# Performance work log

Hardware: AMD Instinct MI355X
Metric: run time of the kernel (lower is better)

Reference implementation:

```python
import jax, jax.numpy as jnp
import numpy as np

NUM_CLASSES = 91
BBOX_XFORM_CLIP = float(np.log(1000.0 / 16.0))
WX, WY, WW, WH = 10.0, 10.0, 5.0, 5.0  # torchvision BoxCoder weights
DETECTIONS_PER_IMG = 100


def _decode_boxes(reg, props):
    # reg: [P, 4*C], props: [P, 4] -> [P, C, 4]  (torchvision BoxCoder.decode)
    widths = props[:, 2] - props[:, 0]
    heights = props[:, 3] - props[:, 1]
    ctr_x = props[:, 0] + 0.5 * widths
    ctr_y = props[:, 1] + 0.5 * heights
    r = reg.reshape(reg.shape[0], -1, 4)
    dx = r[..., 0] / WX
    dy = r[..., 1] / WY
    dw = jnp.minimum(r[..., 2] / WW, BBOX_XFORM_CLIP)
    dh = jnp.minimum(r[..., 3] / WH, BBOX_XFORM_CLIP)
    pcx = dx * widths[:, None] + ctr_x[:, None]
    pcy = dy * heights[:, None] + ctr_y[:, None]
    pw = jnp.exp(dw) * widths[:, None]
    ph = jnp.exp(dh) * heights[:, None]
    return jnp.stack([pcx - 0.5 * pw, pcy - 0.5 * ph, pcx + 0.5 * pw, pcy + 0.5 * ph], axis=-1)


def _clip_boxes(boxes, h, w):
    x = jnp.clip(boxes[..., 0::2], 0.0, float(w))
    y = jnp.clip(boxes[..., 1::2], 0.0, float(h))
    return jnp.stack([x[..., 0], y[..., 0], x[..., 1], y[..., 1]], axis=-1)


def setup_inputs() -> dict:
    key = jax.random.key(0)
    k1, k2, k3, k4, k5 = jax.random.split(key, 5)
    B, P, C, FD = 8, 4096, NUM_CLASSES, 1024
    N = B * P
    class_logits = jax.random.normal(k1, (N, C), dtype=jnp.float32)
    box_regression = 0.5 * jax.random.normal(k2, (N, 4 * C), dtype=jnp.float32)
    # valid proposal boxes inside an 800x800 image: x1<x2, y1<y2
    xy = jax.random.uniform(k3, (N, 2), dtype=jnp.float32) * 700.0
    wh = jax.random.uniform(k4, (N, 2), dtype=jnp.float32) * 96.0 + 4.0
    proposals = jnp.concatenate([xy, xy + wh], axis=-1)
    box_features = jax.random.normal(k5, (N, FD), dtype=jnp.float32)
    return {"class_logits": class_logits, "box_regression": box_regression,
            "proposals": proposals, "box_features": box_features,
            "batch_size": B, "image_h": 800, "image_w": 800}


def reference(class_logits, box_regression, proposals, box_features, batch_size, image_h, image_w):
    B = int(batch_size)
    N = class_logits.shape[0]
    P = N // B
    lg = class_logits.reshape(B, P, NUM_CLASSES)
    rg = box_regression.reshape(B, P, 4 * NUM_CLASSES)
    pr = proposals.reshape(B, P, 4)
    ft = box_features.reshape(B, P, -1)

    def per_image(lg_i, rg_i, pr_i, ft_i):
        boxes = _decode_boxes(rg_i, pr_i)            # [P, C, 4]
        scores = jax.nn.softmax(lg_i, axis=-1)       # [P, C]
        boxes = _clip_boxes(boxes, image_h, image_w)
        boxes = boxes[:, 1:].reshape(-1, 4)          # drop background class -> [P*(C-1), 4]
        scores = scores[:, 1:].reshape(-1)
        # batched_nms with iou_threshold=1.0 never suppresses anything (IoU<=1 always),
        # so keep == indices sorted by score descending, truncated to detections_per_img.
        keep = jnp.argsort(-scores)[:DETECTIONS_PER_IMG]
        boxes = boxes / float(image_h)               # source divides by image_shape[0] only
        kept_boxes = boxes[keep]                     # [D, 4]
        feat_idx = keep // (NUM_CLASSES - 1)         # source: keep / (num_classes-1) int div
        kept_feats = ft_i[feat_idx]                  # [D, FD]
        return kept_boxes, kept_feats

    all_boxes, all_features = jax.vmap(per_image)(lg, rg, pr, ft)
    return all_boxes, all_features
```

## Files before the change

### kernel.cpp

```cpp
#include <hip/hip_runtime.h>
#include <hip/hip_bf16.h>

#define NCLS 91
#define NFG 90
#define NDET 100
#define FDIM 1024
#define CAP 4096
#define NBUK 4096
#define BBOX_CLIP 4.135166556742356f
#define RPB 32

__global__ void k_zero(unsigned* __restrict__ p, int n) {
    int i = blockIdx.x * 256 + threadIdx.x;
    if (i < n) p[i] = 0u;
}

__global__ __launch_bounds__(256) void k_softhist(const float* __restrict__ logits,
                                                  float* __restrict__ rowoff,
                                                  unsigned* __restrict__ ghist, int P) {
    __shared__ unsigned h[NBUK];
    for (int b = threadIdx.x; b < NBUK; b += 256) h[b] = 0u;
    __syncthreads();
    int bpi = (P + RPB - 1) / RPB;
    int img = blockIdx.x / bpi;
    int blk = blockIdx.x % bpi;
    int wave = threadIdx.x >> 6, lane = threadIdx.x & 63;
    #pragma unroll
    for (int it = 0; it < RPB / 4; it++) {
        int rl = blk * RPB + it * 4 + wave;
        if (rl >= P) break;
        long long row = (long long)img * P + rl;
        const float* r = logits + row * NCLS;
        float l1 = r[lane];
        float l2 = (lane < NCLS - 64) ? r[64 + lane] : -INFINITY;
        float m = fmaxf(l1, l2);
        #pragma unroll
        for (int o = 32; o; o >>= 1) m = fmaxf(m, __shfl_xor(m, o));
        float e = expf(l1 - m) + ((lane < NCLS - 64) ? expf(l2 - m) : 0.0f);
        #pragma unroll
        for (int o = 32; o; o >>= 1) e += __shfl_xor(e, o);
        float off = m + logf(e);
        if (lane == 0) rowoff[row] = off;
        if (lane >= 1) {
            unsigned k1 = __float_as_uint(expf(l1 - off));
            atomicAdd(&h[k1 >> 20], 1u);
        }
        if (lane < NCLS - 64) {
            unsigned k2 = __float_as_uint(expf(l2 - off));
            atomicAdd(&h[k2 >> 20], 1u);
        }
    }
    __syncthreads();
    for (int b = threadIdx.x; b < NBUK; b += 256)
        if (h[b]) atomicAdd(&ghist[img * NBUK + b], h[b]);
}

__global__ void k_threshold(const unsigned* __restrict__ ghist,
                            unsigned* __restrict__ lowBound) {
    __shared__ unsigned partial[256];
    __shared__ unsigned suffix[257];
    int img = blockIdx.x;
    const unsigned* h = ghist + img * NBUK;
    unsigned local[16];
    unsigned sum = 0;
    #pragma unroll
    for (int i = 0; i < 16; i++) { local[i] = h[threadIdx.x * 16 + i]; sum += local[i]; }
    partial[threadIdx.x] = sum;
    __syncthreads();
    if (threadIdx.x == 0) {
        unsigned run = 0;
        suffix[256] = 0;
        for (int t = 255; t >= 0; t--) { run += partial[t]; suffix[t] = run; }
    }
    __syncthreads();
    unsigned run = suffix[threadIdx.x + 1];
    #pragma unroll
    for (int i = 15; i >= 0; i--) {
        unsigned prev = run;
        run += local[i];
        if (run >= NDET && prev < NDET)
            lowBound[img] = ((unsigned)(threadIdx.x * 16 + i)) << 20;
    }
}

__global__ void k_collect(const float* __restrict__ logits,
                          const float* __restrict__ rowoff,
                          const unsigned* __restrict__ lowBound,
                          unsigned* __restrict__ gcnt,
                          unsigned long long* __restrict__ cand, int P, int bpi) {
    int img = blockIdx.x / bpi;
    int blk = blockIdx.x % bpi;
    unsigned lb = lowBound[img];
    int base = blk * 4096;
    int rowbase = img * P;
    int elems = P * NFG;
    #pragma unroll
    for (int i = 0; i < 16; i++) {
        int e = base + i * 256 + threadIdx.x;
        if (e < elems) {
            int p = e / NFG, cm = e - p * NFG;
            long long rr = rowbase + p;
            float sc = expf(logits[rr * NCLS + cm + 1] - rowoff[rr]);
            unsigned key = __float_as_uint(sc);
            if (key >= lb) {
                unsigned pos = atomicAdd(&gcnt[img], 1u);
                if (pos < CAP)
                    cand[(long long)img * CAP + pos] =
                        ((unsigned long long)key << 32) | (unsigned)(0xFFFFFFFFu - (unsigned)e);
            }
        }
    }
}

__global__ __launch_bounds__(256) void k_sort_boxes(
        const unsigned long long* __restrict__ cand,
        const unsigned* __restrict__ gcnt,
        const float* __restrict__ reg,
        const float* __restrict__ props,
        const int* __restrict__ pH, const int* __restrict__ pW,
        float* __restrict__ outBoxes, unsigned* __restrict__ keepRow, int P) {
    __shared__ unsigned long long keys[CAP];
    int img = blockIdx.x;
    unsigned cnt = gcnt[img];
    if (cnt > CAP) cnt = CAP;
    int n = 128;
    while (n < (int)cnt) n <<= 1;
    for (int i = threadIdx.x; i < n; i += 256)
        keys[i] = (i < (int)cnt) ? cand[(long long)img * CAP + i] : 0ULL;
    __syncthreads();
    for (int k = 2; k <= n; k <<= 1) {
        for (int j = k >> 1; j > 0; j >>= 1) {
            for (int i = threadIdx.x; i < n; i += 256) {
                int ixj = i ^ j;
                if (ixj > i) {
                    bool up = ((i & k) == 0);
                    unsigned long long a = keys[i], b = keys[ixj];
                    if ((a > b) == up) { keys[i] = b; keys[ixj] = a; }
                }
            }
            __syncthreads();
        }
    }
    if (threadIdx.x < NDET) {
        unsigned long long key = keys[n - 1 - threadIdx.x];
        unsigned e = 0xFFFFFFFFu - (unsigned)(key & 0xFFFFFFFFull);
        int p = e / NFG, cm = e - p * NFG, c = cm + 1;
        long long r = (long long)img * P + p;
        float x1 = props[r * 4 + 0], y1 = props[r * 4 + 1];
        float x2 = props[r * 4 + 2], y2 = props[r * 4 + 3];
        float w = x2 - x1, hgt = y2 - y1;
        float cx = x1 + 0.5f * w, cy = y1 + 0.5f * hgt;
        const float* rr = reg + r * (4 * NCLS) + 4 * c;
        float dx = rr[0] / 10.0f, dy = rr[1] / 10.0f;
        float dw = fminf(rr[2] / 5.0f, BBOX_CLIP);
        float dh = fminf(rr[3] / 5.0f, BBOX_CLIP);
        float pcx = dx * w + cx, pcy = dy * hgt + cy;
        float pw_ = expf(dw) * w, ph_ = expf(dh) * hgt;
        float bx1 = pcx - 0.5f * pw_, by1 = pcy - 0.5f * ph_;
        float bx2 = pcx + 0.5f * pw_, by2 = pcy + 0.5f * ph_;
        float W = (float)(*pW), H = (float)(*pH);
        bx1 = fminf(fmaxf(bx1, 0.0f), W);
        bx2 = fminf(fmaxf(bx2, 0.0f), W);
        by1 = fminf(fmaxf(by1, 0.0f), H);
        by2 = fminf(fmaxf(by2, 0.0f), H);
        int o = (img * NDET + threadIdx.x) * 4;
        outBoxes[o + 0] = bx1 / H;
        outBoxes[o + 1] = by1 / H;
        outBoxes[o + 2] = bx2 / H;
        outBoxes[o + 3] = by2 / H;
        keepRow[img * NDET + threadIdx.x] = (unsigned)r;
    }
}

__global__ void k_feats(const float* __restrict__ feats,
                        const unsigned* __restrict__ keepRow,
                        float* __restrict__ outF) {
    int det = blockIdx.x;
    long long r = keepRow[det];
    const float4* src = (const float4*)(feats + r * FDIM);
    float4* dst = (float4*)(outF + (long long)det * FDIM);
    dst[threadIdx.x] = src[threadIdx.x];
}

extern "C" void kernel_launch(void* const* d_in, const int* in_sizes, int n_in,
                              void* d_out, int out_size, void* d_ws, size_t ws_size,
                              hipStream_t stream) {
    const float* logits = (const float*)d_in[0];
    const float* reg    = (const float*)d_in[1];
    const float* props  = (const float*)d_in[2];
    const float* feats  = (const float*)d_in[3];
    const int*   pH     = (const int*)d_in[5];
    const int*   pW     = (const int*)d_in[6];

    int N = in_sizes[0] / NCLS;
    int B = out_size / (NDET * (4 + FDIM));
    int P = N / B;
    int elems = P * NFG;
    int bpi_hist = (P + RPB - 1) / RPB;
    int bpi_col  = (elems + 4095) / 4096;

    char* ws = (char*)d_ws;
    float* rowoff = (float*)ws;
    unsigned* ghist = (unsigned*)(rowoff + N);
    unsigned* gcnt  = ghist + (size_t)B * NBUK;
    unsigned* lowB  = gcnt + B;
    size_t off = (size_t)N * 4 + (size_t)(B * NBUK + 2 * B) * 4;
    off = (off + 7) & ~(size_t)7;
    unsigned long long* cand = (unsigned long long*)(ws + off);
    unsigned* keepRow = (unsigned*)(cand + (size_t)B * CAP);

    float* outBoxes = (float*)d_out;
    float* outFeats = outBoxes + (size_t)B * NDET * 4;

    int nzero = B * NBUK + B;
    k_zero<<<(nzero + 255) / 256, 256, 0, stream>>>(ghist, nzero);
    k_softhist<<<B * bpi_hist, 256, 0, stream>>>(logits, rowoff, ghist, P);
    k_threshold<<<B, 256, 0, stream>>>(ghist, lowB);
    k_collect<<<B * bpi_col, 256, 0, stream>>>(logits, rowoff, lowB, gcnt, cand, P, bpi_col);
    k_sort_boxes<<<B, 256, 0, stream>>>(cand, gcnt, reg, props, pH, pW, outBoxes, keepRow, P);
    k_feats<<<B * NDET, 256, 0, stream>>>(feats, keepRow, outFeats);
}
```

Measured before the change: 243.1 us.

## Fuse all postprocess stages into one cooperative persistent kernel with grid syncs

```diff
diff --git a/kernel.cpp b/kernel.cpp
--- a/kernel.cpp
+++ b/kernel.cpp
@@ -1,5 +1,8 @@
 #include <hip/hip_runtime.h>
 #include <hip/hip_bf16.h>
+#include <hip/hip_cooperative_groups.h>
+
+namespace cg = cooperative_groups;
 
 #define NCLS 91
 #define NFG 90
@@ -8,29 +11,63 @@
 #define CAP 4096
 #define NBUK 4096
 #define BBOX_CLIP 4.135166556742356f
-#define RPB 32
-
-__global__ void k_zero(unsigned* __restrict__ p, int n) {
-    int i = blockIdx.x * 256 + threadIdx.x;
-    if (i < n) p[i] = 0u;
-}
-
-__global__ __launch_bounds__(256) void k_softhist(const float* __restrict__ logits,
-                                                  float* __restrict__ rowoff,
-                                                  unsigned* __restrict__ ghist, int P) {
-    __shared__ unsigned h[NBUK];
-    for (int b = threadIdx.x; b < NBUK; b += 256) h[b] = 0u;
+#define GRID 256
+#define TPB 256
+#define MAXRPB 512
+
+struct Params {
+    const float* logits; const float* reg; const float* props; const float* feats;
+    const int* pH; const int* pW;
+    unsigned* ghist; unsigned* gcnt; unsigned* lowB;
+    unsigned long long* cand; unsigned* keepRow;
+    float* outBoxes; float* outFeats;
+    int P; int B;
+};
+
+__device__ __forceinline__ unsigned ald(const unsigned* p) {
+    return __hip_atomic_load(p, __ATOMIC_RELAXED, __HIP_MEMORY_SCOPE_AGENT);
+}
+__device__ __forceinline__ void ast(unsigned* p, unsigned v) {
+    __hip_atomic_store(p, v, __ATOMIC_RELAXED, __HIP_MEMORY_SCOPE_AGENT);
+}
+__device__ __forceinline__ unsigned long long ald64(const unsigned long long* p) {
+    return __hip_atomic_load(p, __ATOMIC_RELAXED, __HIP_MEMORY_SCOPE_AGENT);
+}
+__device__ __forceinline__ void ast64(unsigned long long* p, unsigned long long v) {
+    __hip_atomic_store(p, v, __ATOMIC_RELAXED, __HIP_MEMORY_SCOPE_AGENT);
+}
+
+__global__ __launch_bounds__(TPB) void fused_frcnn(Params p) {
+    cg::grid_group grid = cg::this_grid();
+
+    __shared__ unsigned long long smem[CAP];
+    unsigned* hist = (unsigned*)smem;
+    float*    rowf = (float*)(hist + NBUK);
+    unsigned* maxk = (unsigned*)(rowf + MAXRPB);
+    unsigned* tpart = (unsigned*)((char*)smem + 24 * 1024);
+    unsigned* tsuf  = tpart + 256;
+    unsigned long long* keys = smem;
+
+    const int GPB = GRID / p.B;
+    const int img = blockIdx.x / GPB;
+    const int blk = blockIdx.x % GPB;
+    const int rpb = (p.P + GPB - 1) / GPB;
+    const int rpw = (rpb + 3) / 4;
+    const int wave = threadIdx.x >> 6, lane = threadIdx.x & 63;
+    const int gtid = blockIdx.x * TPB + threadIdx.x;
+
+    for (int i = gtid; i < p.B * NBUK; i += GRID * TPB) ast(&p.ghist[i], 0u);
+    if (gtid < p.B) ast(&p.gcnt[gtid], 0u);
+    grid.sync();
+
+    for (int b = threadIdx.x; b < NBUK; b += TPB) hist[b] = 0u;
     __syncthreads();
-    int bpi = (P + RPB - 1) / RPB;
-    int img = blockIdx.x / bpi;
-    int blk = blockIdx.x % bpi;
-    int wave = threadIdx.x >> 6, lane = threadIdx.x & 63;
-    #pragma unroll
-    for (int it = 0; it < RPB / 4; it++) {
-        int rl = blk * RPB + it * 4 + wave;
-        if (rl >= P) break;
-        long long row = (long long)img * P + rl;
-        const float* r = logits + row * NCLS;
+    for (int it = 0; it < rpw; it++) {
+        int lr = wave * rpw + it;
+        int rl = blk * rpb + lr;
+        if (lr >= rpb || lr >= MAXRPB || rl >= p.P) break;
+        long long row = (long long)img * p.P + rl;
+        const float* r = p.logits + row * NCLS;
         float l1 = r[lane];
         float l2 = (lane < NCLS - 64) ? r[64 + lane] : -INFINITY;
         float m = fmaxf(l1, l2);
@@ -40,183 +77,177 @@
         #pragma unroll
         for (int o = 32; o; o >>= 1) e += __shfl_xor(e, o);
         float off = m + logf(e);
-        if (lane == 0) rowoff[row] = off;
-        if (lane >= 1) {
-            unsigned k1 = __float_as_uint(expf(l1 - off));
-            atomicAdd(&h[k1 >> 20], 1u);
-        }
-        if (lane < NCLS - 64) {
-            unsigned k2 = __float_as_uint(expf(l2 - off));
-            atomicAdd(&h[k2 >> 20], 1u);
-        }
+        unsigned k1 = (lane >= 1) ? __float_as_uint(expf(l1 - off)) : 0u;
+        unsigned k2 = (lane < NCLS - 64) ? __float_as_uint(expf(l2 - off)) : 0u;
+        if (lane >= 1)         atomicAdd(&hist[k1 >> 20], 1u);
+        if (lane < NCLS - 64)  atomicAdd(&hist[k2 >> 20], 1u);
+        unsigned km = k1 > k2 ? k1 : k2;
+        #pragma unroll
+        for (int o = 32; o; o >>= 1) { unsigned t = __shfl_xor(km, o); km = km > t ? km : t; }
+        if (lane == 0) { rowf[lr] = off; maxk[lr] = km; }
     }
     __syncthreads();
-    for (int b = threadIdx.x; b < NBUK; b += 256)
-        if (h[b]) atomicAdd(&ghist[img * NBUK + b], h[b]);
-}
-
-__global__ void k_threshold(const unsigned* __restrict__ ghist,
-                            unsigned* __restrict__ lowBound) {
-    __shared__ unsigned partial[256];
-    __shared__ unsigned suffix[257];
-    int img = blockIdx.x;
-    const unsigned* h = ghist + img * NBUK;
-    unsigned local[16];
-    unsigned sum = 0;
-    #pragma unroll
-    for (int i = 0; i < 16; i++) { local[i] = h[threadIdx.x * 16 + i]; sum += local[i]; }
-    partial[threadIdx.x] = sum;
-    __syncthreads();
-    if (threadIdx.x == 0) {
-        unsigned run = 0;
-        suffix[256] = 0;
-        for (int t = 255; t >= 0; t--) { run += partial[t]; suffix[t] = run; }
-    }
-    __syncthreads();
-    unsigned run = suffix[threadIdx.x + 1];
-    #pragma unroll
-    for (int i = 15; i >= 0; i--) {
-        unsigned prev = run;
-        run += local[i];
-        if (run >= NDET && prev < NDET)
-            lowBound[img] = ((unsigned)(threadIdx.x * 16 + i)) << 20;
-    }
-}
-
-__global__ void k_collect(const float* __restrict__ logits,
-                          const float* __restrict__ rowoff,
-                          const unsigned* __restrict__ lowBound,
-                          unsigned* __restrict__ gcnt,
-                          unsigned long long* __restrict__ cand, int P, int bpi) {
-    int img = blockIdx.x / bpi;
-    int blk = blockIdx.x % bpi;
-    unsigned lb = lowBound[img];
-    int base = blk * 4096;
-    int rowbase = img * P;
-    int elems = P * NFG;
-    #pragma unroll
-    for (int i = 0; i < 16; i++) {
-        int e = base + i * 256 + threadIdx.x;
-        if (e < elems) {
-            int p = e / NFG, cm = e - p * NFG;
-            long long rr = rowbase + p;
-            float sc = expf(logits[rr * NCLS + cm + 1] - rowoff[rr]);
-            unsigned key = __float_as_uint(sc);
-            if (key >= lb) {
-                unsigned pos = atomicAdd(&gcnt[img], 1u);
-                if (pos < CAP)
-                    cand[(long long)img * CAP + pos] =
-                        ((unsigned long long)key << 32) | (unsigned)(0xFFFFFFFFu - (unsigned)e);
-            }
-        }
-    }
-}
-
-__global__ __launch_bounds__(256) void k_sort_boxes(
-        const unsigned long long* __restrict__ cand,
-        const unsigned* __restrict__ gcnt,
-        const float* __restrict__ reg,
-        const float* __restrict__ props,
-        const int* __restrict__ pH, const int* __restrict__ pW,
-        float* __restrict__ outBoxes, unsigned* __restrict__ keepRow, int P) {
-    __shared__ unsigned long long keys[CAP];
-    int img = blockIdx.x;
-    unsigned cnt = gcnt[img];
-    if (cnt > CAP) cnt = CAP;
-    int n = 128;
-    while (n < (int)cnt) n <<= 1;
-    for (int i = threadIdx.x; i < n; i += 256)
-        keys[i] = (i < (int)cnt) ? cand[(long long)img * CAP + i] : 0ULL;
-    __syncthreads();
-    for (int k = 2; k <= n; k <<= 1) {
-        for (int j = k >> 1; j > 0; j >>= 1) {
-            for (int i = threadIdx.x; i < n; i += 256) {
-                int ixj = i ^ j;
-                if (ixj > i) {
-                    bool up = ((i & k) == 0);
-                    unsigned long long a = keys[i], b = keys[ixj];
-                    if ((a > b) == up) { keys[i] = b; keys[ixj] = a; }
+    for (int b = threadIdx.x; b < NBUK; b += TPB)
+        if (hist[b]) atomicAdd(&p.ghist[img * NBUK + b], hist[b]);
+    grid.sync();
+
+    if (blockIdx.x < (unsigned)p.B) {
+        const unsigned* h = p.ghist + blockIdx.x * NBUK;
+        unsigned local[16], sum = 0;
+        #pragma unroll
+        for (int i = 0; i < 16; i++) { local[i] = ald(&h[threadIdx.x * 16 + i]); sum += local[i]; }
+        tpart[threadIdx.x] = sum;
+        __syncthreads();
+        if (threadIdx.x == 0) {
+            unsigned run = 0; tsuf[256] = 0;
+            for (int t = 255; t >= 0; t--) { run += tpart[t]; tsuf[t] = run; }
+        }
+        __syncthreads();
+        unsigned run = tsuf[threadIdx.x + 1];
+        #pragma unroll
+        for (int i = 15; i >= 0; i--) {
+            unsigned prev = run; run += local[i];
+            if (run >= NDET && prev < NDET)
+                ast(&p.lowB[blockIdx.x], ((unsigned)(threadIdx.x * 16 + i)) << 20);
+        }
+    }
+    grid.sync();
+
+    {
+        unsigned lb = ald(&p.lowB[img]);
+        for (int it = 0; it < rpw; it++) {
+            int lr = wave * rpw + it;
+            int rl = blk * rpb + lr;
+            if (lr >= rpb || lr >= MAXRPB || rl >= p.P) break;
+            if (maxk[lr] < lb) continue;
+            float off = rowf[lr];
+            long long row = (long long)img * p.P + rl;
+            const float* r = p.logits + row * NCLS;
+            float l1 = r[lane];
+            float l2 = (lane < NCLS - 64) ? r[64 + lane] : -INFINITY;
+            if (lane >= 1) {
+                unsigned k1 = __float_as_uint(expf(l1 - off));
+                if (k1 >= lb) {
+                    unsigned pos = atomicAdd(&p.gcnt[img], 1u);
+                    if (pos < CAP)
+                        ast64(&p.cand[(long long)img * CAP + pos],
+                              ((unsigned long long)k1 << 32) |
+                              (unsigned)(0xFFFFFFFFu - (unsigned)(rl * NFG + lane - 1)));
                 }
             }
+            if (lane < NCLS - 64) {
+                unsigned k2 = __float_as_uint(expf(l2 - off));
+                if (k2 >= lb) {
+                    unsigned pos = atomicAdd(&p.gcnt[img], 1u);
+                    if (pos < CAP)
+                        ast64(&p.cand[(long long)img * CAP + pos],
+                              ((unsigned long long)k2 << 32) |
+                              (unsigned)(0xFFFFFFFFu - (unsigned)(rl * NFG + 63 + lane)));
+                }
+            }
+        }
+    }
+    grid.sync();
+
+    if (blockIdx.x < (unsigned)p.B) {
+        int im = blockIdx.x;
+        unsigned cnt = ald(&p.gcnt[im]);
+        if (cnt > CAP) cnt = CAP;
+        int n = 128;
+        while (n < (int)cnt) n <<= 1;
+        __syncthreads();
+        for (int i = threadIdx.x; i < n; i += TPB)
+            keys[i] = (i < (int)cnt) ? ald64(&p.cand[(long long)im * CAP + i]) : 0ULL;
+        __syncthreads();
+        for (int k = 2; k <= n; k <<= 1) {
+            for (int j = k >> 1; j > 0; j >>= 1) {
+                for (int i = threadIdx.x; i < n; i += TPB) {
+                    int ixj = i ^ j;
+                    if (ixj > i) {
+                        bool up = ((i & k) == 0);
+                        unsigned long long a = keys[i], b = keys[ixj];
+                        if ((a > b) == up) { keys[i] = b; keys[ixj] = a; }
+                    }
+                }
+                __syncthreads();
+            }
+        }
+        if (threadIdx.x < NDET) {
+            unsigned long long key = keys[n - 1 - threadIdx.x];
+            unsigned e = 0xFFFFFFFFu - (unsigned)(key & 0xFFFFFFFFull);
+            int pr = e / NFG, cm = e - pr * NFG, c = cm + 1;
+            long long rw = (long long)im * p.P + pr;
+            float x1 = p.props[rw * 4 + 0], y1 = p.props[rw * 4 + 1];
+            float x2 = p.props[rw * 4 + 2], y2 = p.props[rw * 4 + 3];
+            float w = x2 - x1, hgt = y2 - y1;
+            float cx = x1 + 0.5f * w, cy = y1 + 0.5f * hgt;
+            const float* rr = p.reg + rw * (4 * NCLS) + 4 * c;
+            float dx = rr[0] / 10.0f, dy = rr[1] / 10.0f;
+            float dw = fminf(rr[2] / 5.0f, BBOX_CLIP);
+            float dh = fminf(rr[3] / 5.0f, BBOX_CLIP);
+            float pcx = dx * w + cx, pcy = dy * hgt + cy;
+            float pw_ = expf(dw) * w, ph_ = expf(dh) * hgt;
+            float bx1 = pcx - 0.5f * pw_, by1 = pcy - 0.5f * ph_;
+            float bx2 = pcx + 0.5f * pw_, by2 = pcy + 0.5f * ph_;
+            float W = (float)(*p.pW), H = (float)(*p.pH);
+            bx1 = fminf(fmaxf(bx1, 0.0f), W);
+            bx2 = fminf(fmaxf(bx2, 0.0f), W);
+            by1 = fminf(fmaxf(by1, 0.0f), H);
+            by2 = fminf(fmaxf(by2, 0.0f), H);
+            int o = (im * NDET + threadIdx.x) * 4;
+            p.outBoxes[o + 0] = bx1 / H;
+            p.outBoxes[o + 1] = by1 / H;
+            p.outBoxes[o + 2] = bx2 / H;
+            p.outBoxes[o + 3] = by2 / H;
+            ast(&p.keepRow[im * NDET + threadIdx.x], (unsigned)rw);
+        }
+    }
+    grid.sync();
+
+    {
+        unsigned* bc = (unsigned*)smem;
+        int ndet = p.B * NDET;
+        for (int d = blockIdx.x; d < ndet; d += GRID) {
             __syncthreads();
-        }
-    }
-    if (threadIdx.x < NDET) {
-        unsigned long long key = keys[n - 1 - threadIdx.x];
-        unsigned e = 0xFFFFFFFFu - (unsigned)(key & 0xFFFFFFFFull);
-        int p = e / NFG, cm = e - p * NFG, c = cm + 1;
-        long long r = (long long)img * P + p;
-        float x1 = props[r * 4 + 0], y1 = props[r * 4 + 1];
-        float x2 = props[r * 4 + 2], y2 = props[r * 4 + 3];
-        float w = x2 - x1, hgt = y2 - y1;
-        float cx = x1 + 0.5f * w, cy = y1 + 0.5f * hgt;
-        const float* rr = reg + r * (4 * NCLS) + 4 * c;
-        float dx = rr[0] / 10.0f, dy = rr[1] / 10.0f;
-        float dw = fminf(rr[2] / 5.0f, BBOX_CLIP);
-        float dh = fminf(rr[3] / 5.0f, BBOX_CLIP);
-        float pcx = dx * w + cx, pcy = dy * hgt + cy;
-        float pw_ = expf(dw) * w, ph_ = expf(dh) * hgt;
-        float bx1 = pcx - 0.5f * pw_, by1 = pcy - 0.5f * ph_;
-        float bx2 = pcx + 0.5f * pw_, by2 = pcy + 0.5f * ph_;
-        float W = (float)(*pW), H = (float)(*pH);
-        bx1 = fminf(fmaxf(bx1, 0.0f), W);
-        bx2 = fminf(fmaxf(bx2, 0.0f), W);
-        by1 = fminf(fmaxf(by1, 0.0f), H);
-        by2 = fminf(fmaxf(by2, 0.0f), H);
-        int o = (img * NDET + threadIdx.x) * 4;
-        outBoxes[o + 0] = bx1 / H;
-        outBoxes[o + 1] = by1 / H;
-        outBoxes[o + 2] = bx2 / H;
-        outBoxes[o + 3] = by2 / H;
-        keepRow[img * NDET + threadIdx.x] = (unsigned)r;
-    }
-}
-
-__global__ void k_feats(const float* __restrict__ feats,
-                        const unsigned* __restrict__ keepRow,
-                        float* __restrict__ outF) {
-    int det = blockIdx.x;
-    long long r = keepRow[det];
-    const float4* src = (const float4*)(feats + r * FDIM);
-    float4* dst = (float4*)(outF + (long long)det * FDIM);
-    dst[threadIdx.x] = src[threadIdx.x];
+            if (threadIdx.x == 0) bc[0] = ald(&p.keepRow[d]);
+            __syncthreads();
+            long long rw = bc[0];
+            const float4* src = (const float4*)(p.feats + rw * FDIM);
+            float4* dst = (float4*)(p.outFeats + (long long)d * FDIM);
+            dst[threadIdx.x] = src[threadIdx.x];
+        }
+    }
 }
 
 extern "C" void kernel_launch(void* const* d_in, const int* in_sizes, int n_in,
                               void* d_out, int out_size, void* d_ws, size_t ws_size,
                               hipStream_t stream) {
-    const float* logits = (const float*)d_in[0];
-    const float* reg    = (const float*)d_in[1];
-    const float* props  = (const float*)d_in[2];
-    const float* feats  = (const float*)d_in[3];
-    const int*   pH     = (const int*)d_in[5];
-    const int*   pW     = (const int*)d_in[6];
-
     int N = in_sizes[0] / NCLS;
     int B = out_size / (NDET * (4 + FDIM));
     int P = N / B;
-    int elems = P * NFG;
-    int bpi_hist = (P + RPB - 1) / RPB;
-    int bpi_col  = (elems + 4095) / 4096;
 
     char* ws = (char*)d_ws;
-    float* rowoff = (float*)ws;
-    unsigned* ghist = (unsigned*)(rowoff + N);
+    unsigned* ghist = (unsigned*)ws;
     unsigned* gcnt  = ghist + (size_t)B * NBUK;
     unsigned* lowB  = gcnt + B;
-    size_t off = (size_t)N * 4 + (size_t)(B * NBUK + 2 * B) * 4;
-    off = (off + 7) & ~(size_t)7;
+    size_t off = ((size_t)(B * NBUK + 2 * B) * 4 + 7) & ~(size_t)7;
     unsigned long long* cand = (unsigned long long*)(ws + off);
     unsigned* keepRow = (unsigned*)(cand + (size_t)B * CAP);
 
-    float* outBoxes = (float*)d_out;
-    float* outFeats = outBoxes + (size_t)B * NDET * 4;
-
-    int nzero = B * NBUK + B;
-    k_zero<<<(nzero + 255) / 256, 256, 0, stream>>>(ghist, nzero);
-    k_softhist<<<B * bpi_hist, 256, 0, stream>>>(logits, rowoff, ghist, P);
-    k_threshold<<<B, 256, 0, stream>>>(ghist, lowB);
-    k_collect<<<B * bpi_col, 256, 0, stream>>>(logits, rowoff, lowB, gcnt, cand, P, bpi_col);
-    k_sort_boxes<<<B, 256, 0, stream>>>(cand, gcnt, reg, props, pH, pW, outBoxes, keepRow, P);
-    k_feats<<<B * NDET, 256, 0, stream>>>(feats, keepRow, outFeats);
-}
+    Params prm;
+    prm.logits = (const float*)d_in[0];
+    prm.reg    = (const float*)d_in[1];
+    prm.props  = (const float*)d_in[2];
+    prm.feats  = (const float*)d_in[3];
+    prm.pH     = (const int*)d_in[5];
+    prm.pW     = (const int*)d_in[6];
+    prm.ghist = ghist; prm.gcnt = gcnt; prm.lowB = lowB;
+    prm.cand = cand; prm.keepRow = keepRow;
+    prm.outBoxes = (float*)d_out;
+    prm.outFeats = (float*)d_out + (size_t)B * NDET * 4;
+    prm.P = P; prm.B = B;
+
+    void* args[] = { &prm };
+    hipLaunchCooperativeKernel((void*)fused_frcnn, dim3(GRID), dim3(TPB),
+                               args, 0, stream);
+}
```

Result: slower. 401.7 us (+65.3%).
